# Kernel tuning notes

Hardware: AMD Instinct MI355X
Metric: run time of the kernel (lower is better)

## Reference

```python
import jax, jax.numpy as jnp
import numpy as np

NUM_HEADS = 16
HEAD_DIM = 64
LORA_SCALE = 1.0 / 8.0  # lora_alpha (1) / r (8), loralib defaults


def setup_inputs() -> dict:
    key = jax.random.key(0)
    ks = jax.random.split(key, 10)
    B, N, C = 4, 2048, 1024
    O = 3 * NUM_HEADS * HEAD_DIM  # 3072
    s = lambda fan: 1.0 / np.sqrt(fan)
    return {
        "x": jax.random.normal(ks[0], (B, N, C), jnp.float32),
        "W_qkv": jax.random.normal(ks[1], (O, C), jnp.float32) * s(C),
        "W_lora": jax.random.normal(ks[2], (O, C), jnp.float32) * s(C),
        "b_lora": jax.random.normal(ks[3], (O,), jnp.float32) * s(C),
        "A_q": jax.random.normal(ks[4], (8, C), jnp.float32) * s(C),
        "B_q": jnp.zeros((NUM_HEADS * HEAD_DIM, 8), jnp.float32) + jax.random.normal(ks[5], (NUM_HEADS * HEAD_DIM, 8), jnp.float32) * 0.02,
        "A_v": jax.random.normal(ks[6], (8, C), jnp.float32) * s(C),
        "B_v": jax.random.normal(ks[7], (NUM_HEADS * HEAD_DIM, 8), jnp.float32) * 0.02,
        "W_out": jax.random.normal(ks[8], (C, NUM_HEADS * HEAD_DIM), jnp.float32) * s(NUM_HEADS * HEAD_DIM),
        "b_out": jax.random.normal(ks[9], (C,), jnp.float32) * s(NUM_HEADS * HEAD_DIM),
    }


def reference(x, W_qkv, W_lora, b_lora, A_q, B_q, A_v, B_v, W_out, b_out):
    B, N, C = x.shape
    H, D = NUM_HEADS, HEAD_DIM
    scale = D ** (-0.5)

    def split_qkv(t):
        t = t.reshape(B, N, 3, H, D).transpose(2, 0, 3, 1, 4)
        return t[0], t[1], t[2]

    q, k, v = split_qkv(jnp.einsum('bnc,oc->bno', x, W_qkv))
    ql, _, vl = split_qkv(jnp.einsum('bnc,oc->bno', x, W_lora) + b_lora)

    # low-rank LoRA updates for Q and V slices only (K disabled)
    dq = (jnp.einsum('bnc,rc->bnr', x, A_q) @ B_q.T) * LORA_SCALE  # (B,N,HD)
    dv = (jnp.einsum('bnc,rc->bnr', x, A_v) @ B_v.T) * LORA_SCALE
    dq = dq.reshape(B, N, H, D).transpose(0, 2, 1, 3)
    dv = dv.reshape(B, N, H, D).transpose(0, 2, 1, 3)

    q = q + ql + dq
    v = v + vl + dv

    attn = jax.nn.softmax(jnp.einsum('bhnd,bhmd->bhnm', q, k) * scale, axis=-1)
    out = jnp.einsum('bhnm,bhmd->bhnd', attn, v)
    out = out.transpose(0, 2, 1, 3).reshape(B, N, H * D)  # b h n d -> b n (h d)
    return jnp.einsum('bnk,ck->bnc', out, W_out) + b_out
```

## Files before the change

kernel.cpp:

```cpp
#include <hip/hip_runtime.h>
#include <hip/hip_bf16.h>

typedef unsigned short u16;
typedef unsigned int u32;
typedef __attribute__((ext_vector_type(8))) short bf16x8;
typedef __attribute__((ext_vector_type(4))) float f32x4;
typedef __attribute__((ext_vector_type(16))) float f32x16;

#define GLDS16(gptr, lptr)                                                        \
  __builtin_amdgcn_global_load_lds(                                               \
      (__attribute__((address_space(1))) const void*)(gptr),                      \
      (__attribute__((address_space(3))) void*)(lptr), 16, 0, 0)

__device__ __forceinline__ u16 f2bf(float f) {
  union { float f; unsigned u; } v; v.f = f;
  unsigned r = v.u + 0x7fffu + ((v.u >> 16) & 1u);
  return (u16)(r >> 16);
}

__device__ __forceinline__ u32 pack_bf2(float a, float b) {
  union { __hip_bfloat162 h2; u32 u; } v;
  v.h2 = __float22bfloat162_rn(make_float2(a, b));
  return v.u;
}

__global__ void k_prep(const float* __restrict__ x, const float* __restrict__ Wqkv,
                       const float* __restrict__ Wlora, const float* __restrict__ blora,
                       const float* __restrict__ Aq, const float* __restrict__ Bq,
                       const float* __restrict__ Av, const float* __restrict__ Bv,
                       const float* __restrict__ Wout,
                       u16* __restrict__ Xb, u16* __restrict__ Weff,
                       float* __restrict__ beff, u16* __restrict__ Woutb) {
  const int bid = blockIdx.x, tid = threadIdx.x;
  if (bid < 8192) {
    int i = bid * 256 + tid;
    float4 f = reinterpret_cast<const float4*>(x)[i];
    ushort4 u;
    u.x = f2bf(f.x); u.y = f2bf(f.y); u.z = f2bf(f.z); u.w = f2bf(f.w);
    reinterpret_cast<ushort4*>(Xb)[i] = u;
  } else if (bid < 9216) {
    int i = (bid - 8192) * 256 + tid;
    float4 f = reinterpret_cast<const float4*>(Wout)[i];
    ushort4 u;
    u.x = f2bf(f.x); u.y = f2bf(f.y); u.z = f2bf(f.z); u.w = f2bf(f.w);
    reinterpret_cast<ushort4*>(Woutb)[i] = u;
  } else {
    int idx = (bid - 9216) * 256 + tid;
    int o = idx >> 10, c = idx & 1023;
    float w = Wqkv[idx];
    if (o < 1024) {
      float lr = 0.f;
#pragma unroll
      for (int r = 0; r < 8; ++r) lr += Bq[o * 8 + r] * Aq[r * 1024 + c];
      w += Wlora[idx] + 0.125f * lr;
    } else if (o >= 2048) {
      int o2 = o - 2048;
      float lr = 0.f;
#pragma unroll
      for (int r = 0; r < 8; ++r) lr += Bv[o2 * 8 + r] * Av[r * 1024 + c];
      w += Wlora[idx] + 0.125f * lr;
    }
    Weff[idx] = f2bf(w);
    if (c == 0) beff[o] = (o < 1024 || o >= 2048) ? blora[o] : 0.f;
  }
}

__global__ __launch_bounds__(512, 2)
void k_gemm_qkv(const u16* __restrict__ Xb, const u16* __restrict__ Weff,
                const float* __restrict__ beff, u16* __restrict__ Y) {
  __shared__ u16 As[2 * 256 * 64], Bs[2 * 256 * 64];
  const int tid = threadIdx.x, lane = tid & 63, wave = tid >> 6;
  const int lr = lane & 15, lg = (lane >> 4) & 3;
  const int wr = wave >> 2, wc = wave & 3;
  const int wg = blockIdx.x + 12 * blockIdx.y;
  const int swz = (wg & 7) * 48 + (wg >> 3);
  const int m0 = (swz / 12) * 256, n0 = (swz % 12) * 256;

  const int srow = wave * 8 + (lane >> 3);
  const int schunk = lane & 7;
  f32x4 acc[8][4] = {};

  auto stage = [&](int kt, int bb) {
    const int k0 = kt * 64;
    const int lb = bb * 16384 + (wave * 8) * 64;
#pragma unroll
    for (int i = 0; i < 4; ++i) {
      int row = i * 64 + srow;
      int gc = (schunk ^ (row & 7)) << 3;
      GLDS16(Xb   + (size_t)(m0 + row) * 1024 + k0 + gc, &As[lb + i * 4096]);
      GLDS16(Weff + (size_t)(n0 + row) * 1024 + k0 + gc, &Bs[lb + i * 4096]);
    }
  };

  stage(0, 0);
  stage(1, 1);
  asm volatile("s_waitcnt vmcnt(8)" ::: "memory");
  __builtin_amdgcn_s_barrier();

  for (int kt = 0; kt < 16; ++kt) {
    const int cur = kt & 1;
    const int abase = cur * 16384, bbase = cur * 16384;
#pragma unroll
    for (int mh = 0; mh < 2; ++mh) {
      bf16x8 af[4][2];
#pragma unroll
      for (int mi = 0; mi < 4; ++mi)
#pragma unroll
        for (int kk = 0; kk < 2; ++kk)
          af[mi][kk] = *reinterpret_cast<const bf16x8*>(
              &As[abase + (wr * 128 + (mh * 4 + mi) * 16 + lr) * 64 + (((kk * 4 + lg) ^ (lr & 7)) << 3)]);
#pragma unroll
      for (int nh = 0; nh < 2; ++nh) {
        bf16x8 bf[2][2];
#pragma unroll
        for (int ni = 0; ni < 2; ++ni)
#pragma unroll
          for (int kk = 0; kk < 2; ++kk)
            bf[ni][kk] = *reinterpret_cast<const bf16x8*>(
                &Bs[bbase + (wc * 64 + (nh * 2 + ni) * 16 + lr) * 64 + (((kk * 4 + lg) ^ (lr & 7)) << 3)]);
        __builtin_amdgcn_s_setprio(1);
#pragma unroll
        for (int mi = 0; mi < 4; ++mi)
#pragma unroll
          for (int ni = 0; ni < 2; ++ni)
#pragma unroll
            for (int kk = 0; kk < 2; ++kk)
              acc[mh * 4 + mi][nh * 2 + ni] = __builtin_amdgcn_mfma_f32_16x16x32_bf16(
                  af[mi][kk], bf[ni][kk], acc[mh * 4 + mi][nh * 2 + ni], 0, 0, 0);
        __builtin_amdgcn_s_setprio(0);
        __builtin_amdgcn_sched_barrier(0);
      }
    }
    if (kt == 15) break;
    __builtin_amdgcn_s_barrier();
    if (kt + 2 < 16) {
      stage(kt + 2, cur);
      asm volatile("s_waitcnt vmcnt(8)" ::: "memory");
    } else {
      asm volatile("s_waitcnt vmcnt(0)" ::: "memory");
    }
    __builtin_amdgcn_s_barrier();
  }

#pragma unroll
  for (int mi = 0; mi < 8; ++mi) {
    int row = m0 + wr * 128 + mi * 16 + (lg << 2);
#pragma unroll
    for (int ni = 0; ni < 4; ++ni) {
      int col = n0 + wc * 64 + ni * 16 + lr;
      float bias = beff[col];
      bool isq = col < 1024;
#pragma unroll
      for (int j = 0; j < 4; ++j) {
        float v = acc[mi][ni][j] + bias;
        if (isq) v *= 0.18033688011112042f;
        Y[(size_t)(row + j) * 3072 + col] = f2bf(v);
      }
    }
  }
}

__global__ __launch_bounds__(256)
void k_vtrans(const u16* __restrict__ Y, u16* __restrict__ Vt) {
  __shared__ u16 Ls[64 * 65];
  const int t = threadIdx.x;
  const int bh = blockIdx.y, b = bh >> 4, h = bh & 15;
  const int n0 = blockIdx.x * 64;
#pragma unroll
  for (int c = 0; c < 2; ++c) {
    int idx = c * 256 + t;
    int nl = idx >> 3, d0 = (idx & 7) * 8;
    bf16x8 val = *reinterpret_cast<const bf16x8*>(
        Y + (size_t)(b * 2048 + n0 + nl) * 3072 + 2048 + h * 64 + d0);
#pragma unroll
    for (int j = 0; j < 8; ++j) Ls[(d0 + j) * 65 + nl] = (u16)val[j];
  }
  __syncthreads();
#pragma unroll
  for (int c = 0; c < 2; ++c) {
    int idx = c * 256 + t;
    int dl = idx >> 3, nn = (idx & 7) * 8;
    bf16x8 outv;
#pragma unroll
    for (int j = 0; j < 8; ++j) outv[j] = (short)Ls[dl * 65 + nn + j];
    *reinterpret_cast<bf16x8*>(Vt + (size_t)(bh * 64 + dl) * 2048 + n0 + nn) = outv;
  }
}

__global__ __launch_bounds__(256, 3)
void k_attn(const u16* __restrict__ Y, const u16* __restrict__ Vt, u16* __restrict__ Oa) {
  __shared__ u16 Ks[2][64 * 64], Vs[2][64 * 64];
  const int tid = threadIdx.x, lane = tid & 63, wave = tid >> 6;
  const int b = blockIdx.y >> 4, h = blockIdx.y & 15;
  const int q0 = blockIdx.x * 128;
  const int l31 = lane & 31, hi = lane >> 5;
  const size_t bq = (size_t)b * 2048;
  const size_t bv = (size_t)b * 1024 + h * 64;
  const int hc = h * 64;

  bf16x8 qb[4];
  {
    const u16* yr = Y + (bq + q0 + wave * 32 + l31) * 3072 + hc + hi * 8;
#pragma unroll
    for (int ks = 0; ks < 4; ++ks)
      qb[ks] = *reinterpret_cast<const bf16x8*>(yr + ks * 16);
  }

  float m_run = -1e30f, l_run = 0.f;
  f32x16 oacc[2] = {};

  const int sr = tid >> 3, sc = tid & 7;
  auto stage = [&](int key0, int bb) {
#pragma unroll
    for (int i = 0; i < 2; ++i) {
      int r = i * 32 + sr;
      int gc = (sc ^ (r & 7)) << 3;
      GLDS16(Y + (bq + key0 + r) * 3072 + 1024 + hc + gc, &Ks[bb][i * 2048 + wave * 512]);
      GLDS16(Vt + (bv + r) * 2048 + key0 + gc,            &Vs[bb][i * 2048 + wave * 512]);
    }
  };

  stage(0, 0);
  for (int kt = 0; kt < 32; ++kt) {
    const int cur = kt & 1;
    if (kt < 31) {
      stage((kt + 1) * 64, cur ^ 1);
      asm volatile("s_waitcnt vmcnt(4)" ::: "memory");
    } else {
      asm volatile("s_waitcnt vmcnt(0)" ::: "memory");
    }
    __builtin_amdgcn_s_barrier();
    asm volatile("" ::: "memory");

    bf16x8 kb[2][4], vb[2][4];
#pragma unroll
    for (int t = 0; t < 2; ++t) {
      const u16* kbase = &Ks[cur][(t * 32 + l31) * 64];
      int rx = (t * 32 + l31) & 7;
#pragma unroll
      for (int ks = 0; ks < 4; ++ks)
        kb[t][ks] = *reinterpret_cast<const bf16x8*>(kbase + (((ks * 2 + hi) ^ rx) << 3));
    }
#pragma unroll
    for (int dt = 0; dt < 2; ++dt) {
      const u16* vbase = &Vs[cur][(dt * 32 + l31) * 64];
      int rx = (dt * 32 + l31) & 7;
#pragma unroll
      for (int ks = 0; ks < 4; ++ks)
        vb[dt][ks] = *reinterpret_cast<const bf16x8*>(vbase + (((ks * 2 + hi) ^ rx) << 3));
    }

    f32x16 p4[2] = {};
    __builtin_amdgcn_s_setprio(1);
#pragma unroll
    for (int t = 0; t < 2; ++t)
#pragma unroll
      for (int ks = 0; ks < 4; ++ks)
        p4[t] = __builtin_amdgcn_mfma_f32_32x32x16_bf16(kb[t][ks], qb[ks], p4[t], 0, 0, 0);
    __builtin_amdgcn_s_setprio(0);

    float mx[8];
#pragma unroll
    for (int r = 0; r < 8; ++r)
      mx[r] = fmaxf(fmaxf(p4[0][r], p4[0][r + 8]), fmaxf(p4[1][r], p4[1][r + 8]));
#pragma unroll
    for (int s = 4; s > 0; s >>= 1)
#pragma unroll
      for (int r = 0; r < s; ++r) mx[r] = fmaxf(mx[r], mx[r + s]);
    float tmax = fmaxf(mx[0], __shfl_xor(mx[0], 32));

    if (__any(tmax > m_run + 11.0f)) {
      float mnew = fmaxf(m_run, tmax);
      float alpha = __builtin_amdgcn_exp2f(m_run - mnew);
      m_run = mnew;
      l_run *= alpha;
#pragma unroll
      for (int r = 0; r < 16; ++r) {
        float ab = __shfl(alpha, (r & 3) + 8 * (r >> 2) + 4 * hi);
        oacc[0][r] *= ab;
        oacc[1][r] *= ab;
      }
    }

    float rs = 0.f;
    u32 w[2][4][2];
#pragma unroll
    for (int t = 0; t < 2; ++t)
#pragma unroll
      for (int g = 0; g < 4; ++g) {
        float e0 = __builtin_amdgcn_exp2f(p4[t][4 * g + 0] - m_run);
        float e1 = __builtin_amdgcn_exp2f(p4[t][4 * g + 1] - m_run);
        float e2 = __builtin_amdgcn_exp2f(p4[t][4 * g + 2] - m_run);
        float e3 = __builtin_amdgcn_exp2f(p4[t][4 * g + 3] - m_run);
        rs += (e0 + e1) + (e2 + e3);
        w[t][g][0] = pack_bf2(e0, e1);
        w[t][g][1] = pack_bf2(e2, e3);
      }
    rs += __shfl_xor(rs, 32);
    l_run += rs;

    bf16x8 pa[4];
#pragma unroll
    for (int ks = 0; ks < 4; ++ks) {
      const int t = ks >> 1, q2 = (ks & 1) * 2;
      auto s0 = __builtin_amdgcn_permlane32_swap(w[t][q2][0], w[t][q2 + 1][0], false, false);
      auto s1 = __builtin_amdgcn_permlane32_swap(w[t][q2][1], w[t][q2 + 1][1], false, false);
      union { u32 u[4]; bf16x8 v; } cv;
      cv.u[0] = s0[0]; cv.u[1] = s1[0]; cv.u[2] = s0[1]; cv.u[3] = s1[1];
      pa[ks] = cv.v;
    }

    __builtin_amdgcn_s_setprio(1);
#pragma unroll
    for (int ks = 0; ks < 4; ++ks) {
      oacc[0] = __builtin_amdgcn_mfma_f32_32x32x16_bf16(pa[ks], vb[0][ks], oacc[0], 0, 0, 0);
      oacc[1] = __builtin_amdgcn_mfma_f32_32x32x16_bf16(pa[ks], vb[1][ks], oacc[1], 0, 0, 0);
    }
    __builtin_amdgcn_s_setprio(0);

    asm volatile("" ::: "memory");
    __builtin_amdgcn_s_barrier();
  }

  float linv = __builtin_amdgcn_rcpf(l_run);
  const size_t orow0 = bq + q0 + wave * 32;
#pragma unroll
  for (int r = 0; r < 16; ++r) {
    int qr = (r & 3) + 8 * (r >> 2) + 4 * hi;
    float li = __shfl(linv, qr);
    size_t rb = (orow0 + qr) * 1024 + hc + l31;
    Oa[rb]      = f2bf(oacc[0][r] * li);
    Oa[rb + 32] = f2bf(oacc[1][r] * li);
  }
}

__global__ __launch_bounds__(256, 3)
void k_gemm_out(const u16* __restrict__ Ob, const u16* __restrict__ Wb,
                const float* __restrict__ bout, float* __restrict__ out) {
  __shared__ u16 As[128 * 32], Bs[128 * 32];
  const int tid = threadIdx.x, lane = tid & 63, wave = tid >> 6;
  const int lr = lane & 15, lg = lane >> 4;
  const int wr = wave >> 1, wc = wave & 1;
  const int wg = blockIdx.x + 8 * blockIdx.y;
  const int swz = (wg & 7) * 64 + (wg >> 3);
  const int m0 = (swz >> 3) * 128, n0 = (swz & 7) * 128;
  f32x4 acc[4][4] = {};

  for (int k0 = 0; k0 < 1024; k0 += 32) {
#pragma unroll
    for (int i = 0; i < 2; ++i) {
      int gc = ((tid & 3) ^ ((tid >> 2) & 3)) << 3;
      GLDS16(Ob + (size_t)(m0 + i * 64 + (tid >> 2)) * 1024 + k0 + gc, As + i * 2048 + wave * 512);
      GLDS16(Wb + (size_t)(n0 + i * 64 + (tid >> 2)) * 1024 + k0 + gc, Bs + i * 2048 + wave * 512);
    }
    __syncthreads();
    bf16x8 af[4], bfr[4];
#pragma unroll
    for (int t = 0; t < 4; ++t) {
      int ch = ((lg ^ (lr & 3)) & 3) << 3;
      af[t]  = *reinterpret_cast<const bf16x8*>(As + (wr * 64 + t * 16 + lr) * 32 + ch);
      bfr[t] = *reinterpret_cast<const bf16x8*>(Bs + (wc * 64 + t * 16 + lr) * 32 + ch);
    }
#pragma unroll
    for (int mi = 0; mi < 4; ++mi)
#pragma unroll
      for (int ni = 0; ni < 4; ++ni)
        acc[mi][ni] = __builtin_amdgcn_mfma_f32_16x16x32_bf16(af[mi], bfr[ni], acc[mi][ni], 0, 0, 0);
    __syncthreads();
  }

#pragma unroll
  for (int mi = 0; mi < 4; ++mi) {
    int row = m0 + wr * 64 + mi * 16 + (lg << 2);
#pragma unroll
    for (int ni = 0; ni < 4; ++ni) {
      int col = n0 + wc * 64 + ni * 16 + lr;
      float bias = bout[col];
#pragma unroll
      for (int j = 0; j < 4; ++j)
        out[(size_t)(row + j) * 1024 + col] = acc[mi][ni][j] + bias;
    }
  }
}

extern "C" void kernel_launch(void* const* d_in, const int* in_sizes, int n_in,
                              void* d_out, int out_size, void* d_ws, size_t ws_size,
                              hipStream_t stream) {
  const float* x     = (const float*)d_in[0];
  const float* Wqkv  = (const float*)d_in[1];
  const float* Wlora = (const float*)d_in[2];
  const float* blora = (const float*)d_in[3];
  const float* Aq    = (const float*)d_in[4];
  const float* Bq    = (const float*)d_in[5];
  const float* Av    = (const float*)d_in[6];
  const float* Bv    = (const float*)d_in[7];
  const float* Wout  = (const float*)d_in[8];
  const float* bout  = (const float*)d_in[9];
  float* out = (float*)d_out;

  char* w = (char*)d_ws;
  auto alloc = [&](size_t bytes) { char* p = w; w += (bytes + 255) & ~(size_t)255; return p; };
  u16*   Xb    = (u16*)alloc((size_t)8192 * 1024 * 2);
  u16*   Weff  = (u16*)alloc((size_t)3072 * 1024 * 2);
  float* beff  = (float*)alloc((size_t)3072 * 4);
  u16*   Woutb = (u16*)alloc((size_t)1024 * 1024 * 2);
  u16*   Y     = (u16*)alloc((size_t)8192 * 3072 * 2);
  u16*   Vt    = (u16*)alloc((size_t)4096 * 1024 * 2 * 2);
  u16*   Oa    = Xb;

  k_prep<<<dim3(21504), dim3(256), 0, stream>>>(x, Wqkv, Wlora, blora, Aq, Bq, Av, Bv, Wout,
                                                Xb, Weff, beff, Woutb);
  k_gemm_qkv<<<dim3(12, 32), dim3(512), 0, stream>>>(Xb, Weff, beff, Y);
  k_vtrans<<<dim3(32, 64), dim3(256), 0, stream>>>(Y, Vt);
  k_attn<<<dim3(16, 64), dim3(256), 0, stream>>>(Y, Vt, Oa);
  k_gemm_out<<<dim3(8, 64), dim3(256), 0, stream>>>(Oa, Woutb, bout, out);
}
```

Measured before the change: 336.6 us.

## Fuse V transpose into QKV GEMM epilogue and pipeline output GEMM

The QKV GEMM tile shrinks from 256x256 to 256x128, so V-column tiles can transpose their results through LDS and write Vt directly. This removes the separate k_vtrans kernel and its round trip of V through global memory. The output projection GEMM is rebuilt to match the QKV kernel: 512 threads, 256x128 tiles, K-step 64 and double-buffered async global-to-LDS loads. Smaller QKV tiles reuse less data per block and require twice as many blocks.

```diff
diff --git a/kernel.cpp b/kernel.cpp
--- a/kernel.cpp
+++ b/kernel.cpp
@@ -67,123 +67,120 @@
 
 __global__ __launch_bounds__(512, 2)
 void k_gemm_qkv(const u16* __restrict__ Xb, const u16* __restrict__ Weff,
-                const float* __restrict__ beff, u16* __restrict__ Y) {
-  __shared__ u16 As[2 * 256 * 64], Bs[2 * 256 * 64];
+                const float* __restrict__ beff, u16* __restrict__ Y, u16* __restrict__ Vt) {
+  __shared__ u16 SH[49152];
   const int tid = threadIdx.x, lane = tid & 63, wave = tid >> 6;
   const int lr = lane & 15, lg = (lane >> 4) & 3;
-  const int wr = wave >> 2, wc = wave & 3;
-  const int wg = blockIdx.x + 12 * blockIdx.y;
-  const int swz = (wg & 7) * 48 + (wg >> 3);
-  const int m0 = (swz / 12) * 256, n0 = (swz % 12) * 256;
-
-  const int srow = wave * 8 + (lane >> 3);
-  const int schunk = lane & 7;
-  f32x4 acc[8][4] = {};
+  const int wr = wave >> 1, wc = wave & 1;
+  const int wg = blockIdx.x;
+  const int swz = (wg & 7) * 96 + (wg >> 3);
+  const int m0 = (swz / 24) * 256, n0 = (swz % 24) * 128;
 
   auto stage = [&](int kt, int bb) {
     const int k0 = kt * 64;
-    const int lb = bb * 16384 + (wave * 8) * 64;
+    const int r8 = tid >> 3, ch = tid & 7;
 #pragma unroll
     for (int i = 0; i < 4; ++i) {
-      int row = i * 64 + srow;
-      int gc = (schunk ^ (row & 7)) << 3;
-      GLDS16(Xb   + (size_t)(m0 + row) * 1024 + k0 + gc, &As[lb + i * 4096]);
-      GLDS16(Weff + (size_t)(n0 + row) * 1024 + k0 + gc, &Bs[lb + i * 4096]);
+      int row = i * 64 + r8;
+      int gc = (ch ^ (row & 7)) << 3;
+      GLDS16(Xb + (size_t)(m0 + row) * 1024 + k0 + gc, &SH[bb * 16384 + (i * 64 + wave * 8) * 64]);
+    }
+#pragma unroll
+    for (int i = 0; i < 2; ++i) {
+      int row = i * 64 + r8;
+      int gc = (ch ^ (row & 7)) << 3;
+      GLDS16(Weff + (size_t)(n0 + row) * 1024 + k0 + gc,
+             &SH[32768 + bb * 8192 + (i * 64 + wave * 8) * 64]);
     }
   };
 
+  f32x4 acc[4][4] = {};
   stage(0, 0);
   stage(1, 1);
-  asm volatile("s_waitcnt vmcnt(8)" ::: "memory");
+  asm volatile("s_waitcnt vmcnt(6)" ::: "memory");
   __builtin_amdgcn_s_barrier();
 
   for (int kt = 0; kt < 16; ++kt) {
     const int cur = kt & 1;
-    const int abase = cur * 16384, bbase = cur * 16384;
-#pragma unroll
-    for (int mh = 0; mh < 2; ++mh) {
-      bf16x8 af[4][2];
-#pragma unroll
-      for (int mi = 0; mi < 4; ++mi)
+    const u16* Ab = &SH[cur * 16384];
+    const u16* Bb = &SH[32768 + cur * 8192];
+    bf16x8 afr[4][2], bfr[4][2];
+#pragma unroll
+    for (int mi = 0; mi < 4; ++mi)
+#pragma unroll
+      for (int kk = 0; kk < 2; ++kk)
+        afr[mi][kk] = *reinterpret_cast<const bf16x8*>(
+            &Ab[(wr * 64 + mi * 16 + lr) * 64 + (((kk * 4 + lg) ^ (lr & 7)) << 3)]);
+#pragma unroll
+    for (int ni = 0; ni < 4; ++ni)
+#pragma unroll
+      for (int kk = 0; kk < 2; ++kk)
+        bfr[ni][kk] = *reinterpret_cast<const bf16x8*>(
+            &Bb[(wc * 64 + ni * 16 + lr) * 64 + (((kk * 4 + lg) ^ (lr & 7)) << 3)]);
+    __builtin_amdgcn_s_setprio(1);
+#pragma unroll
+    for (int mi = 0; mi < 4; ++mi)
+#pragma unroll
+      for (int ni = 0; ni < 4; ++ni)
 #pragma unroll
         for (int kk = 0; kk < 2; ++kk)
-          af[mi][kk] = *reinterpret_cast<const bf16x8*>(
-              &As[abase + (wr * 128 + (mh * 4 + mi) * 16 + lr) * 64 + (((kk * 4 + lg) ^ (lr & 7)) << 3)]);
-#pragma unroll
-      for (int nh = 0; nh < 2; ++nh) {
-        bf16x8 bf[2][2];
-#pragma unroll
-        for (int ni = 0; ni < 2; ++ni)
-#pragma unroll
-          for (int kk = 0; kk < 2; ++kk)
-            bf[ni][kk] = *reinterpret_cast<const bf16x8*>(
-                &Bs[bbase + (wc * 64 + (nh * 2 + ni) * 16 + lr) * 64 + (((kk * 4 + lg) ^ (lr & 7)) << 3)]);
-        __builtin_amdgcn_s_setprio(1);
-#pragma unroll
-        for (int mi = 0; mi < 4; ++mi)
-#pragma unroll
-          for (int ni = 0; ni < 2; ++ni)
-#pragma unroll
-            for (int kk = 0; kk < 2; ++kk)
-              acc[mh * 4 + mi][nh * 2 + ni] = __builtin_amdgcn_mfma_f32_16x16x32_bf16(
-                  af[mi][kk], bf[ni][kk], acc[mh * 4 + mi][nh * 2 + ni], 0, 0, 0);
-        __builtin_amdgcn_s_setprio(0);
-        __builtin_amdgcn_sched_barrier(0);
-      }
-    }
+          acc[mi][ni] = __builtin_amdgcn_mfma_f32_16x16x32_bf16(
+              afr[mi][kk], bfr[ni][kk], acc[mi][ni], 0, 0, 0);
+    __builtin_amdgcn_s_setprio(0);
     if (kt == 15) break;
     __builtin_amdgcn_s_barrier();
     if (kt + 2 < 16) {
       stage(kt + 2, cur);
-      asm volatile("s_waitcnt vmcnt(8)" ::: "memory");
+      asm volatile("s_waitcnt vmcnt(6)" ::: "memory");
     } else {
       asm volatile("s_waitcnt vmcnt(0)" ::: "memory");
     }
     __builtin_amdgcn_s_barrier();
   }
 
-#pragma unroll
-  for (int mi = 0; mi < 8; ++mi) {
-    int row = m0 + wr * 128 + mi * 16 + (lg << 2);
-#pragma unroll
-    for (int ni = 0; ni < 4; ++ni) {
-      int col = n0 + wc * 64 + ni * 16 + lr;
-      float bias = beff[col];
-      bool isq = col < 1024;
-#pragma unroll
-      for (int j = 0; j < 4; ++j) {
-        float v = acc[mi][ni][j] + bias;
-        if (isq) v *= 0.18033688011112042f;
-        Y[(size_t)(row + j) * 3072 + col] = f2bf(v);
+  if (n0 < 2048) {
+#pragma unroll
+    for (int mi = 0; mi < 4; ++mi) {
+      int row = m0 + wr * 64 + mi * 16 + (lg << 2);
+#pragma unroll
+      for (int ni = 0; ni < 4; ++ni) {
+        int col = n0 + wc * 64 + ni * 16 + lr;
+        float bias = beff[col];
+        bool isq = col < 1024;
+#pragma unroll
+        for (int j = 0; j < 4; ++j) {
+          float v = acc[mi][ni][j] + bias;
+          if (isq) v *= 0.18033688011112042f;
+          Y[(size_t)(row + j) * 3072 + col] = f2bf(v);
+        }
       }
     }
-  }
-}
-
-__global__ __launch_bounds__(256)
-void k_vtrans(const u16* __restrict__ Y, u16* __restrict__ Vt) {
-  __shared__ u16 Ls[64 * 65];
-  const int t = threadIdx.x;
-  const int bh = blockIdx.y, b = bh >> 4, h = bh & 15;
-  const int n0 = blockIdx.x * 64;
-#pragma unroll
-  for (int c = 0; c < 2; ++c) {
-    int idx = c * 256 + t;
-    int nl = idx >> 3, d0 = (idx & 7) * 8;
-    bf16x8 val = *reinterpret_cast<const bf16x8*>(
-        Y + (size_t)(b * 2048 + n0 + nl) * 3072 + 2048 + h * 64 + d0);
-#pragma unroll
-    for (int j = 0; j < 8; ++j) Ls[(d0 + j) * 65 + nl] = (u16)val[j];
-  }
-  __syncthreads();
-#pragma unroll
-  for (int c = 0; c < 2; ++c) {
-    int idx = c * 256 + t;
-    int dl = idx >> 3, nn = (idx & 7) * 8;
-    bf16x8 outv;
-#pragma unroll
-    for (int j = 0; j < 8; ++j) outv[j] = (short)Ls[dl * 65 + nn + j];
-    *reinterpret_cast<bf16x8*>(Vt + (size_t)(bh * 64 + dl) * 2048 + n0 + nn) = outv;
+  } else {
+    __syncthreads();
+    u32* L32 = reinterpret_cast<u32*>(SH);
+#pragma unroll
+    for (int mi = 0; mi < 4; ++mi) {
+      int tok = wr * 64 + mi * 16 + (lg << 2);
+#pragma unroll
+      for (int ni = 0; ni < 4; ++ni) {
+        int hd_l = wc * 64 + ni * 16 + lr;
+        float bias = beff[n0 + hd_l];
+        L32[hd_l * 130 + (tok >> 1)]     = pack_bf2(acc[mi][ni][0] + bias, acc[mi][ni][1] + bias);
+        L32[hd_l * 130 + (tok >> 1) + 1] = pack_bf2(acc[mi][ni][2] + bias, acc[mi][ni][3] + bias);
+      }
+    }
+    __syncthreads();
+    const int b = m0 >> 11, tok0 = m0 & 2047;
+    const int hdb = n0 - 2048;
+#pragma unroll
+    for (int p = 0; p < 8; ++p) {
+      int idx = p * 512 + tid;
+      int hd_l = idx >> 5, c = idx & 31;
+      uint2 d0 = *reinterpret_cast<uint2*>(&L32[hd_l * 130 + c * 4]);
+      uint2 d1 = *reinterpret_cast<uint2*>(&L32[hd_l * 130 + c * 4 + 2]);
+      *reinterpret_cast<uint4*>(&Vt[((size_t)(b * 1024 + hdb + hd_l)) * 2048 + tok0 + c * 8]) =
+          make_uint4(d0.x, d0.y, d1.x, d1.y);
+    }
   }
 }
 
@@ -334,39 +331,77 @@
   }
 }
 
-__global__ __launch_bounds__(256, 3)
+__global__ __launch_bounds__(512, 2)
 void k_gemm_out(const u16* __restrict__ Ob, const u16* __restrict__ Wb,
                 const float* __restrict__ bout, float* __restrict__ out) {
-  __shared__ u16 As[128 * 32], Bs[128 * 32];
+  __shared__ u16 SH[49152];
   const int tid = threadIdx.x, lane = tid & 63, wave = tid >> 6;
-  const int lr = lane & 15, lg = lane >> 4;
+  const int lr = lane & 15, lg = (lane >> 4) & 3;
   const int wr = wave >> 1, wc = wave & 1;
-  const int wg = blockIdx.x + 8 * blockIdx.y;
-  const int swz = (wg & 7) * 64 + (wg >> 3);
-  const int m0 = (swz >> 3) * 128, n0 = (swz & 7) * 128;
+  const int wg = blockIdx.x;
+  const int swz = (wg & 7) * 32 + (wg >> 3);
+  const int m0 = (swz >> 3) * 256, n0 = (swz & 7) * 128;
+
+  auto stage = [&](int kt, int bb) {
+    const int k0 = kt * 64;
+    const int r8 = tid >> 3, ch = tid & 7;
+#pragma unroll
+    for (int i = 0; i < 4; ++i) {
+      int row = i * 64 + r8;
+      int gc = (ch ^ (row & 7)) << 3;
+      GLDS16(Ob + (size_t)(m0 + row) * 1024 + k0 + gc, &SH[bb * 16384 + (i * 64 + wave * 8) * 64]);
+    }
+#pragma unroll
+    for (int i = 0; i < 2; ++i) {
+      int row = i * 64 + r8;
+      int gc = (ch ^ (row & 7)) << 3;
+      GLDS16(Wb + (size_t)(n0 + row) * 1024 + k0 + gc,
+             &SH[32768 + bb * 8192 + (i * 64 + wave * 8) * 64]);
+    }
+  };
+
   f32x4 acc[4][4] = {};
-
-  for (int k0 = 0; k0 < 1024; k0 += 32) {
-#pragma unroll
-    for (int i = 0; i < 2; ++i) {
-      int gc = ((tid & 3) ^ ((tid >> 2) & 3)) << 3;
-      GLDS16(Ob + (size_t)(m0 + i * 64 + (tid >> 2)) * 1024 + k0 + gc, As + i * 2048 + wave * 512);
-      GLDS16(Wb + (size_t)(n0 + i * 64 + (tid >> 2)) * 1024 + k0 + gc, Bs + i * 2048 + wave * 512);
-    }
-    __syncthreads();
-    bf16x8 af[4], bfr[4];
-#pragma unroll
-    for (int t = 0; t < 4; ++t) {
-      int ch = ((lg ^ (lr & 3)) & 3) << 3;
-      af[t]  = *reinterpret_cast<const bf16x8*>(As + (wr * 64 + t * 16 + lr) * 32 + ch);
-      bfr[t] = *reinterpret_cast<const bf16x8*>(Bs + (wc * 64 + t * 16 + lr) * 32 + ch);
-    }
+  stage(0, 0);
+  stage(1, 1);
+  asm volatile("s_waitcnt vmcnt(6)" ::: "memory");
+  __builtin_amdgcn_s_barrier();
+
+  for (int kt = 0; kt < 16; ++kt) {
+    const int cur = kt & 1;
+    const u16* Ab = &SH[cur * 16384];
+    const u16* Bb = &SH[32768 + cur * 8192];
+    bf16x8 afr[4][2], bfr[4][2];
 #pragma unroll
     for (int mi = 0; mi < 4; ++mi)
 #pragma unroll
+      for (int kk = 0; kk < 2; ++kk)
+        afr[mi][kk] = *reinterpret_cast<const bf16x8*>(
+            &Ab[(wr * 64 + mi * 16 + lr) * 64 + (((kk * 4 + lg) ^ (lr & 7)) << 3)]);
+#pragma unroll
+    for (int ni = 0; ni < 4; ++ni)
+#pragma unroll
+      for (int kk = 0; kk < 2; ++kk)
+        bfr[ni][kk] = *reinterpret_cast<const bf16x8*>(
+            &Bb[(wc * 64 + ni * 16 + lr) * 64 + (((kk * 4 + lg) ^ (lr & 7)) << 3)]);
+    __builtin_amdgcn_s_setprio(1);
+#pragma unroll
+    for (int mi = 0; mi < 4; ++mi)
+#pragma unroll
       for (int ni = 0; ni < 4; ++ni)
-        acc[mi][ni] = __builtin_amdgcn_mfma_f32_16x16x32_bf16(af[mi], bfr[ni], acc[mi][ni], 0, 0, 0);
-    __syncthreads();
+#pragma unroll
+        for (int kk = 0; kk < 2; ++kk)
+          acc[mi][ni] = __builtin_amdgcn_mfma_f32_16x16x32_bf16(
+              afr[mi][kk], bfr[ni][kk], acc[mi][ni], 0, 0, 0);
+    __builtin_amdgcn_s_setprio(0);
+    if (kt == 15) break;
+    __builtin_amdgcn_s_barrier();
+    if (kt + 2 < 16) {
+      stage(kt + 2, cur);
+      asm volatile("s_waitcnt vmcnt(6)" ::: "memory");
+    } else {
+      asm volatile("s_waitcnt vmcnt(0)" ::: "memory");
+    }
+    __builtin_amdgcn_s_barrier();
   }
 
 #pragma unroll
@@ -410,8 +445,7 @@
 
   k_prep<<<dim3(21504), dim3(256), 0, stream>>>(x, Wqkv, Wlora, blora, Aq, Bq, Av, Bv, Wout,
                                                 Xb, Weff, beff, Woutb);
-  k_gemm_qkv<<<dim3(12, 32), dim3(512), 0, stream>>>(Xb, Weff, beff, Y);
-  k_vtrans<<<dim3(32, 64), dim3(256), 0, stream>>>(Y, Vt);
+  k_gemm_qkv<<<dim3(768), dim3(512), 0, stream>>>(Xb, Weff, beff, Y, Vt);
   k_attn<<<dim3(16, 64), dim3(256), 0, stream>>>(Y, Vt, Oa);
-  k_gemm_out<<<dim3(8, 64), dim3(256), 0, stream>>>(Oa, Woutb, bout, out);
-}
+  k_gemm_out<<<dim3(256), dim3(512), 0, stream>>>(Oa, Woutb, bout, out);
+}
```

Result: faster. 314.1 us (-6.7%).
